# Performance work log

Measured on AMD Instinct MI355X. Metric: run time of the kernel, lower is better.

## Reference

```python
import jax, jax.numpy as jnp
import numpy as np

LAYERS = [3, 1024, 512, 256, 128, 1]
WIDTHS = [3, 1024, 1024, 1024, 1024, 1]  # width per BsPINN: 2^(i-1)*Layers[i]
N = 131072


def _mask(num_blocks, bs1, bs2):
    # block-diagonal mask of ones, built statically (constant under jit)
    return jnp.asarray(np.kron(np.eye(num_blocks, dtype=np.float32),
                               np.ones((bs1, bs2), dtype=np.float32)))


def _xavier(key, shape, fan_in, fan_out):
    lim = np.sqrt(6.0 / (fan_in + fan_out)).astype(np.float32)
    return jax.random.uniform(key, shape, jnp.float32, -lim, lim)


def setup_inputs() -> dict:
    key = jax.random.key(0)
    ks = jax.random.split(key, 6)
    inp = {
        "X": jax.random.uniform(ks[0], (N, 3), dtype=jnp.float32),
        "lb_X": jnp.zeros((3,), jnp.float32),
        "ub_X": jnp.ones((3,), jnp.float32),
    }
    for i in range(5):
        # xavier scale per sub-block Layers[i] x Layers[i+1], as in the torch init
        inp[f"W{i}"] = _xavier(ks[i + 1], (WIDTHS[i], WIDTHS[i + 1]),
                               LAYERS[i], LAYERS[i + 1])
        inp[f"b{i}"] = jnp.zeros((1, WIDTHS[i + 1]), jnp.float32)
    return inp


def reference(X, lb_X, ub_X, W0, b0, W1, b1, W2, b2, W3, b3, W4, b4):
    # masks for hidden layers l=2,3: 2 blocks of 512x512, 4 blocks of 256x256
    m2 = _mask(2, LAYERS[2], 2 * LAYERS[3])   # [1024,1024]
    m3 = _mask(4, LAYERS[3], 2 * LAYERS[4])   # [1024,1024]
    h = 2.0 * (X - lb_X) / (ub_X - lb_X) - 1.0  # [N,3]
    h = jnp.sin(h @ W0 + b0)            # [N,1024] dense
    h = jnp.sin(h @ W1 + b1)            # [N,1024] dense
    h = jnp.sin(h @ (W2 * m2) + b2)     # [N,1024] block-diag (2 blocks)
    h = jnp.sin(h @ (W3 * m3) + b3)     # [N,1024] block-diag (4 blocks)
    return h @ W4 + b4                  # [N,1]
```

## Files before the change

kernel.cpp:

```cpp
#include <hip/hip_runtime.h>

typedef _Float16 f16x8 __attribute__((ext_vector_type(8)));
typedef _Float16 f16x4 __attribute__((ext_vector_type(4)));
typedef __fp16  fp16x2 __attribute__((ext_vector_type(2)));
typedef float f32x4 __attribute__((ext_vector_type(4)));
typedef unsigned int u32;

#define N_TOTAL 131072
#define INV2PI 0.15915494309189535f

__device__ __forceinline__ float fast_sin_revs(float t) {
  return __builtin_amdgcn_sinf(__builtin_amdgcn_fractf(t));
}

__global__ __launch_bounds__(512) void pack_weights(
    const float* __restrict__ W1, const float* __restrict__ W2,
    const float* __restrict__ W3, _Float16* __restrict__ WF1,
    _Float16* __restrict__ WF2, _Float16* __restrict__ WF3) {
  int t = blockIdx.x * 512 + threadIdx.x;
  const float* src; _Float16* dst; int idx, ct, kt, lane, kbase;
  if (t < 131072) {
    idx = t; src = W1; dst = WF1;
    ct = idx >> 11; kt = (idx >> 6) & 31; lane = idx & 63; kbase = 0;
  } else if (t < 196608) {
    idx = t - 131072; src = W2; dst = WF2;
    ct = idx >> 10; kt = (idx >> 6) & 15; lane = idx & 63;
    kbase = (ct >= 32) ? 512 : 0;
  } else {
    idx = t - 196608; src = W3; dst = WF3;
    ct = idx >> 9; kt = (idx >> 6) & 7; lane = idx & 63;
    kbase = (ct >> 4) << 8;
  }
  int c  = ct * 16 + (lane & 15);
  int k0 = kbase + kt * 32 + ((lane >> 4) << 3);
  f16x8 v;
#pragma unroll
  for (int j = 0; j < 8; ++j) v[j] = (_Float16)src[(size_t)(k0 + j) * 1024 + c];
  *reinterpret_cast<f16x8*>(dst + (size_t)idx * 8) = v;
}

template <int KTFULL>
__device__ __forceinline__ void kloop(const _Float16* __restrict__ WF, char* hbr,
                                      f32x4 (&acc)[4][4], int ct0, int lane,
                                      int nkt, int ktW0, u32 ldsk0) {
  const f16x8* wf = reinterpret_cast<const f16x8*>(WF);
  const int arow = lane & 15;
  const int koff = (lane >> 4) << 3;
  const u32 abase = (u32)(arow * 1024);
  const u32 axor  = (u32)((arow & 7) << 4);
  const u32 wbase = (u32)((ct0 * KTFULL + ktW0) * 64 + lane);
#pragma unroll 1
  for (int kt = 0; kt < nkt; ++kt) {
    f16x8 w[4];
#pragma unroll
    for (int cf = 0; cf < 4; ++cf)
      w[cf] = wf[wbase + (u32)(cf * KTFULL) * 64u + (u32)kt * 64u];
    u32 kb = ldsk0 + (u32)(kt * 64) + (u32)(koff * 2);
    f16x8 h[4];
#pragma unroll
    for (int rf = 0; rf < 4; ++rf) {
      u32 addr = ((u32)(rf * 16384) + abase + kb) ^ axor;
      h[rf] = *reinterpret_cast<const f16x8*>(hbr + addr);
    }
    __builtin_amdgcn_s_setprio(1);
#pragma unroll
    for (int cf = 0; cf < 4; ++cf)
#pragma unroll
      for (int rf = 0; rf < 4; ++rf)
        acc[cf][rf] = __builtin_amdgcn_mfma_f32_16x16x32_f16(w[cf], h[rf],
                                                             acc[cf][rf], 0, 0, 0);
    __builtin_amdgcn_s_setprio(0);
  }
}

__global__
__attribute__((amdgpu_flat_work_group_size(1024, 1024), amdgpu_waves_per_eu(4, 4)))
void bspinn_fused(
    const float* __restrict__ X, const float* __restrict__ lb,
    const float* __restrict__ ub,
    const float* __restrict__ W0, const float* __restrict__ b0,
    const _Float16* __restrict__ WF1, const float* __restrict__ b1,
    const _Float16* __restrict__ WF2, const float* __restrict__ b2,
    const _Float16* __restrict__ WF3, const float* __restrict__ b3,
    const float* __restrict__ W4, float* __restrict__ P) {
  __shared__ alignas(16) char hb[128 * 1024];
  __shared__ float xs[128 * 4];
  __shared__ float partials[16 * 128];

  const int tid  = threadIdx.x;
  const int lane = tid & 63;
  const int wid  = tid >> 6;
  const int tile = blockIdx.x >> 1;
  const int half = blockIdx.x & 1;
  const int r0   = tile * 128;

  if (tid < 384) {
    int r = tid / 3, j = tid - r * 3;
    float x = X[(size_t)r0 * 3 + tid];
    xs[r * 4 + j] = 2.0f * (x - lb[j]) / (ub[j] - lb[j]) - 1.0f;
  }

  const int cwave = wid & 7;
  const int rgrp  = wid >> 3;
  char* hbr = hb + rgrp * (64 * 1024);
  const int ct0 = half * 32 + cwave * 4;

  auto layer1 = [&](int cbase) {
    int c1 = tid & 511;
    int rb = (tid >> 9) * 64;
    int cg = cbase + c1;
    float w0v = W0[cg] * INV2PI, w1v = W0[1024 + cg] * INV2PI;
    float w2v = W0[2048 + cg] * INV2PI, bv = b0[cg] * INV2PI;
#pragma unroll 4
    for (int rr = 0; rr < 64; ++rr) {
      int r = rb + rr;
      float x0 = xs[r * 4], x1 = xs[r * 4 + 1], x2 = xs[r * 4 + 2];
      float v = fast_sin_revs(fmaf(x2, w2v, fmaf(x1, w1v, fmaf(x0, w0v, bv))));
      u32 addr = ((u32)(r * 1024 + c1 * 2)) ^ ((u32)((r & 7) << 4));
      *reinterpret_cast<_Float16*>(hb + addr) = (_Float16)v;
    }
  };

  f32x4 acc[4][4];
  auto zacc = [&]() {
#pragma unroll
    for (int cf = 0; cf < 4; ++cf)
#pragma unroll
      for (int rf = 0; rf < 4; ++rf) acc[cf][rf] = f32x4{0.f, 0.f, 0.f, 0.f};
  };

  auto epi = [&](const float* bias) {
    const int csub = (lane >> 4) << 2;
    const int rr = lane & 15;
#pragma unroll
    for (int cf = 0; cf < 4; ++cf) {
      int cg = half * 512 + cwave * 64 + cf * 16 + csub;
      int cl = cwave * 64 + cf * 16 + csub;
      f32x4 bb = *reinterpret_cast<const f32x4*>(bias + cg);
      f32x4 bc;
#pragma unroll
      for (int i = 0; i < 4; ++i) bc[i] = bb[i] * INV2PI;
#pragma unroll
      for (int rf = 0; rf < 4; ++rf) {
        int r = rf * 16 + rr;
        float s0 = fast_sin_revs(fmaf(acc[cf][rf][0], INV2PI, bc[0]));
        float s1 = fast_sin_revs(fmaf(acc[cf][rf][1], INV2PI, bc[1]));
        float s2 = fast_sin_revs(fmaf(acc[cf][rf][2], INV2PI, bc[2]));
        float s3 = fast_sin_revs(fmaf(acc[cf][rf][3], INV2PI, bc[3]));
        union { fp16x2 h2[2]; f16x4 v; } pk;
        pk.h2[0] = __builtin_amdgcn_cvt_pkrtz(s0, s1);
        pk.h2[1] = __builtin_amdgcn_cvt_pkrtz(s2, s3);
        u32 addr = ((u32)(r * 1024 + cl * 2)) ^ ((u32)((r & 7) << 4));
        *reinterpret_cast<f16x4*>(hbr + addr) = pk.v;
      }
    }
  };

  __syncthreads();
  layer1(0);
  __syncthreads();

  zacc();
  kloop<32>(WF1, hbr, acc, ct0, lane, 16, 0, 0);
  __syncthreads();
  layer1(512);
  __syncthreads();
  kloop<32>(WF1, hbr, acc, ct0, lane, 16, 16, 0);
  __syncthreads();
  epi(b1);
  __syncthreads();

  zacc();
  kloop<16>(WF2, hbr, acc, ct0, lane, 16, 0, 0);
  __syncthreads();
  epi(b2);
  __syncthreads();

  zacc();
  kloop<8>(WF3, hbr, acc, ct0, lane, 8, 0, (u32)((cwave >> 2) * 512));
  __syncthreads();
  epi(b3);
  __syncthreads();

  {
    int seg = wid;
    u32 xr = (u32)((lane & 7) << 4);
    float s0 = 0.f, s1 = 0.f;
#pragma unroll
    for (int kk = 0; kk < 32; kk += 8) {
      int kl = seg * 32 + kk;
      const float* w4p = W4 + half * 512 + kl;
      f16x8 v0 = *reinterpret_cast<const f16x8*>(hb + (((u32)(lane * 1024 + kl * 2)) ^ xr));
      f16x8 v1 = *reinterpret_cast<const f16x8*>(hb + (((u32)((lane + 64) * 1024 + kl * 2)) ^ xr));
#pragma unroll
      for (int j = 0; j < 8; ++j) {
        float wv = w4p[j];
        s0 = fmaf((float)v0[j], wv, s0);
        s1 = fmaf((float)v1[j], wv, s1);
      }
    }
    partials[seg * 128 + lane]      = s0;
    partials[seg * 128 + lane + 64] = s1;
  }
  __syncthreads();
  if (tid < 128) {
    float s = 0.f;
#pragma unroll
    for (int g = 0; g < 16; ++g) s += partials[g * 128 + tid];
    P[(size_t)half * N_TOTAL + r0 + tid] = s;
  }
}

__global__ __launch_bounds__(256) void reduce_out(
    const float* __restrict__ P, const float* __restrict__ b4,
    float* __restrict__ out) {
  int i = blockIdx.x * 256 + threadIdx.x;
  out[i] = P[i] + P[N_TOTAL + i] + b4[0];
}

extern "C" void kernel_launch(void* const* d_in, const int* in_sizes, int n_in,
                              void* d_out, int out_size, void* d_ws, size_t ws_size,
                              hipStream_t stream) {
  const float* X  = (const float*)d_in[0];
  const float* lb = (const float*)d_in[1];
  const float* ub = (const float*)d_in[2];
  const float* W0 = (const float*)d_in[3];
  const float* b0 = (const float*)d_in[4];
  const float* W1 = (const float*)d_in[5];
  const float* b1 = (const float*)d_in[6];
  const float* W2 = (const float*)d_in[7];
  const float* b2 = (const float*)d_in[8];
  const float* W3 = (const float*)d_in[9];
  const float* b3 = (const float*)d_in[10];
  const float* W4 = (const float*)d_in[11];
  const float* b4 = (const float*)d_in[12];
  float* out = (float*)d_out;

  _Float16* WF1 = (_Float16*)d_ws;
  _Float16* WF2 = (_Float16*)((char*)d_ws + 2097152);
  _Float16* WF3 = (_Float16*)((char*)d_ws + 3145728);
  float*    P   = (float*)((char*)d_ws + 3670016);

  hipLaunchKernelGGL(pack_weights, dim3(448), dim3(512), 0, stream,
                     W1, W2, W3, WF1, WF2, WF3);
  hipLaunchKernelGGL(bspinn_fused, dim3((N_TOTAL / 128) * 2), dim3(1024), 0, stream,
                     X, lb, ub, W0, b0, WF1, b1, WF2, b2, WF3, b3, W4, P);
  hipLaunchKernelGGL(reduce_out, dim3(N_TOTAL / 256), dim3(256), 0, stream,
                     P, b4, out);
}
```

Baseline: 528.7 us.

## Split fused MLP into 64-row, 512-thread blocks with cheaper sine and swizzle

Halves the work-group from 128 rows and 1024 threads to 64 rows and 512 threads, using 64KB of LDS. This lets two independent blocks share a CU so their barrier phases can overlap instead of all 16 waves stalling on one barrier. It also replaces the fract-plus-scaled-sin sequence with __sinf on the raw argument, widens the LDS XOR swizzle to 16 rows, and writes layer-1 activations as packed half pairs. Dropping the fract range reduction may cost accuracy for large pre-activations, and each block now reuses the global weight traffic across fewer rows.

Measured after the change: 482.6 us, median of 2. -8.7%, faster.

```diff
diff --git a/kernel.cpp b/kernel.cpp
--- a/kernel.cpp
+++ b/kernel.cpp
@@ -7,11 +7,6 @@
 typedef unsigned int u32;
 
 #define N_TOTAL 131072
-#define INV2PI 0.15915494309189535f
-
-__device__ __forceinline__ float fast_sin_revs(float t) {
-  return __builtin_amdgcn_sinf(__builtin_amdgcn_fractf(t));
-}
 
 __global__ __launch_bounds__(512) void pack_weights(
     const float* __restrict__ W1, const float* __restrict__ W2,
@@ -40,27 +35,28 @@
 }
 
 template <int KTFULL>
-__device__ __forceinline__ void kloop(const _Float16* __restrict__ WF, char* hbr,
+__device__ __forceinline__ void kloop(const _Float16* __restrict__ WF, char* hb,
                                       f32x4 (&acc)[4][4], int ct0, int lane,
                                       int nkt, int ktW0, u32 ldsk0) {
-  const f16x8* wf = reinterpret_cast<const f16x8*>(WF);
+  const f16x8* wf = reinterpret_cast<const f16x8*>(WF) +
+                    (u32)((ct0 * KTFULL + ktW0) * 64 + lane);
   const int arow = lane & 15;
   const int koff = (lane >> 4) << 3;
   const u32 abase = (u32)(arow * 1024);
-  const u32 axor  = (u32)((arow & 7) << 4);
-  const u32 wbase = (u32)((ct0 * KTFULL + ktW0) * 64 + lane);
+  const u32 axor  = (u32)(arow << 4);
+
 #pragma unroll 1
   for (int kt = 0; kt < nkt; ++kt) {
     f16x8 w[4];
 #pragma unroll
     for (int cf = 0; cf < 4; ++cf)
-      w[cf] = wf[wbase + (u32)(cf * KTFULL) * 64u + (u32)kt * 64u];
+      w[cf] = wf[(u32)(cf * KTFULL) * 64u + (u32)kt * 64u];
     u32 kb = ldsk0 + (u32)(kt * 64) + (u32)(koff * 2);
     f16x8 h[4];
 #pragma unroll
     for (int rf = 0; rf < 4; ++rf) {
       u32 addr = ((u32)(rf * 16384) + abase + kb) ^ axor;
-      h[rf] = *reinterpret_cast<const f16x8*>(hbr + addr);
+      h[rf] = *reinterpret_cast<const f16x8*>(hb + addr);
     }
     __builtin_amdgcn_s_setprio(1);
 #pragma unroll
@@ -74,7 +70,7 @@
 }
 
 __global__
-__attribute__((amdgpu_flat_work_group_size(1024, 1024), amdgpu_waves_per_eu(4, 4)))
+__attribute__((amdgpu_flat_work_group_size(512, 512), amdgpu_waves_per_eu(4, 4)))
 void bspinn_fused(
     const float* __restrict__ X, const float* __restrict__ lb,
     const float* __restrict__ ub,
@@ -83,130 +79,122 @@
     const _Float16* __restrict__ WF2, const float* __restrict__ b2,
     const _Float16* __restrict__ WF3, const float* __restrict__ b3,
     const float* __restrict__ W4, float* __restrict__ P) {
-  __shared__ alignas(16) char hb[128 * 1024];
-  __shared__ float xs[128 * 4];
-  __shared__ float partials[16 * 128];
+  __shared__ alignas(16) char hb[64 * 1024];
+  __shared__ float xs[64 * 4];
+  __shared__ float partials[8 * 64];
 
   const int tid  = threadIdx.x;
   const int lane = tid & 63;
   const int wid  = tid >> 6;
   const int tile = blockIdx.x >> 1;
   const int half = blockIdx.x & 1;
-  const int r0   = tile * 128;
-
-  if (tid < 384) {
+  const int r0   = tile * 64;
+
+  if (tid < 192) {
     int r = tid / 3, j = tid - r * 3;
     float x = X[(size_t)r0 * 3 + tid];
     xs[r * 4 + j] = 2.0f * (x - lb[j]) / (ub[j] - lb[j]) - 1.0f;
   }
-
-  const int cwave = wid & 7;
-  const int rgrp  = wid >> 3;
-  char* hbr = hb + rgrp * (64 * 1024);
-  const int ct0 = half * 32 + cwave * 4;
+  __syncthreads();
 
   auto layer1 = [&](int cbase) {
-    int c1 = tid & 511;
-    int rb = (tid >> 9) * 64;
-    int cg = cbase + c1;
-    float w0v = W0[cg] * INV2PI, w1v = W0[1024 + cg] * INV2PI;
-    float w2v = W0[2048 + cg] * INV2PI, bv = b0[cg] * INV2PI;
+    int c0l = (tid & 255) * 2;
+    int rb  = (tid >> 8) * 32;
+    int cg  = cbase + c0l;
+    float wa0 = W0[cg],        wb0 = W0[cg + 1];
+    float wa1 = W0[1024 + cg], wb1 = W0[1025 + cg];
+    float wa2 = W0[2048 + cg], wb2 = W0[2049 + cg];
+    float ba = b0[cg], bbv = b0[cg + 1];
 #pragma unroll 4
-    for (int rr = 0; rr < 64; ++rr) {
-      int r = rb + rr;
+    for (int rr2 = 0; rr2 < 32; ++rr2) {
+      int r = rb + rr2;
       float x0 = xs[r * 4], x1 = xs[r * 4 + 1], x2 = xs[r * 4 + 2];
-      float v = fast_sin_revs(fmaf(x2, w2v, fmaf(x1, w1v, fmaf(x0, w0v, bv))));
-      u32 addr = ((u32)(r * 1024 + c1 * 2)) ^ ((u32)((r & 7) << 4));
-      *reinterpret_cast<_Float16*>(hb + addr) = (_Float16)v;
+      float va = __sinf(fmaf(x2, wa2, fmaf(x1, wa1, fmaf(x0, wa0, ba))));
+      float vb = __sinf(fmaf(x2, wb2, fmaf(x1, wb1, fmaf(x0, wb0, bbv))));
+      union { fp16x2 h2; u32 u; } pk;
+      pk.h2 = __builtin_amdgcn_cvt_pkrtz(va, vb);
+      u32 addr = ((u32)(r * 1024 + c0l * 2)) ^ ((u32)((r & 15) << 4));
+      *reinterpret_cast<u32*>(hb + addr) = pk.u;
     }
   };
 
+  const int csub = (lane >> 4) << 2;
+  const int rr   = lane & 15;
+  const int ct0  = half * 32 + wid * 4;
   f32x4 acc[4][4];
+
   auto zacc = [&]() {
 #pragma unroll
     for (int cf = 0; cf < 4; ++cf)
 #pragma unroll
       for (int rf = 0; rf < 4; ++rf) acc[cf][rf] = f32x4{0.f, 0.f, 0.f, 0.f};
   };
-
-  auto epi = [&](const float* bias) {
-    const int csub = (lane >> 4) << 2;
-    const int rr = lane & 15;
+  auto epi_store = [&](const float* bias) {
 #pragma unroll
     for (int cf = 0; cf < 4; ++cf) {
-      int cg = half * 512 + cwave * 64 + cf * 16 + csub;
-      int cl = cwave * 64 + cf * 16 + csub;
+      int c0l = wid * 64 + cf * 16 + csub;
+      int cg  = half * 512 + c0l;
       f32x4 bb = *reinterpret_cast<const f32x4*>(bias + cg);
-      f32x4 bc;
-#pragma unroll
-      for (int i = 0; i < 4; ++i) bc[i] = bb[i] * INV2PI;
 #pragma unroll
       for (int rf = 0; rf < 4; ++rf) {
         int r = rf * 16 + rr;
-        float s0 = fast_sin_revs(fmaf(acc[cf][rf][0], INV2PI, bc[0]));
-        float s1 = fast_sin_revs(fmaf(acc[cf][rf][1], INV2PI, bc[1]));
-        float s2 = fast_sin_revs(fmaf(acc[cf][rf][2], INV2PI, bc[2]));
-        float s3 = fast_sin_revs(fmaf(acc[cf][rf][3], INV2PI, bc[3]));
+        float s0 = __sinf(acc[cf][rf][0] + bb[0]);
+        float s1 = __sinf(acc[cf][rf][1] + bb[1]);
+        float s2 = __sinf(acc[cf][rf][2] + bb[2]);
+        float s3 = __sinf(acc[cf][rf][3] + bb[3]);
         union { fp16x2 h2[2]; f16x4 v; } pk;
         pk.h2[0] = __builtin_amdgcn_cvt_pkrtz(s0, s1);
         pk.h2[1] = __builtin_amdgcn_cvt_pkrtz(s2, s3);
-        u32 addr = ((u32)(r * 1024 + cl * 2)) ^ ((u32)((r & 7) << 4));
-        *reinterpret_cast<f16x4*>(hbr + addr) = pk.v;
+        u32 addr = ((u32)(r * 1024 + c0l * 2)) ^ ((u32)(rr << 4));
+        *reinterpret_cast<f16x4*>(hb + addr) = pk.v;
       }
     }
   };
 
-  __syncthreads();
   layer1(0);
   __syncthreads();
-
   zacc();
-  kloop<32>(WF1, hbr, acc, ct0, lane, 16, 0, 0);
+  kloop<32>(WF1, hb, acc, ct0, lane, 16, 0, 0);
   __syncthreads();
   layer1(512);
   __syncthreads();
-  kloop<32>(WF1, hbr, acc, ct0, lane, 16, 16, 0);
-  __syncthreads();
-  epi(b1);
+  kloop<32>(WF1, hb, acc, ct0, lane, 16, 16, 0);
+  __syncthreads();
+  epi_store(b1);
   __syncthreads();
 
   zacc();
-  kloop<16>(WF2, hbr, acc, ct0, lane, 16, 0, 0);
-  __syncthreads();
-  epi(b2);
+  kloop<16>(WF2, hb, acc, ct0, lane, 16, 0, 0);
+  __syncthreads();
+  epi_store(b2);
   __syncthreads();
 
   zacc();
-  kloop<8>(WF3, hbr, acc, ct0, lane, 8, 0, (u32)((cwave >> 2) * 512));
-  __syncthreads();
-  epi(b3);
+  kloop<8>(WF3, hb, acc, ct0, lane, 8, 0, (u32)((wid >> 2) * 512));
+  __syncthreads();
+  epi_store(b3);
   __syncthreads();
 
   {
-    int seg = wid;
-    u32 xr = (u32)((lane & 7) << 4);
-    float s0 = 0.f, s1 = 0.f;
-#pragma unroll
-    for (int kk = 0; kk < 32; kk += 8) {
-      int kl = seg * 32 + kk;
+    int r = lane;
+    u32 rb = (u32)(r * 1024);
+    u32 xr = (u32)((r & 15) << 4);
+    float s = 0.f;
+#pragma unroll
+    for (int kk = 0; kk < 64; kk += 8) {
+      int kl = wid * 64 + kk;
       const float* w4p = W4 + half * 512 + kl;
-      f16x8 v0 = *reinterpret_cast<const f16x8*>(hb + (((u32)(lane * 1024 + kl * 2)) ^ xr));
-      f16x8 v1 = *reinterpret_cast<const f16x8*>(hb + (((u32)((lane + 64) * 1024 + kl * 2)) ^ xr));
-#pragma unroll
-      for (int j = 0; j < 8; ++j) {
-        float wv = w4p[j];
-        s0 = fmaf((float)v0[j], wv, s0);
-        s1 = fmaf((float)v1[j], wv, s1);
-      }
-    }
-    partials[seg * 128 + lane]      = s0;
-    partials[seg * 128 + lane + 64] = s1;
-  }
-  __syncthreads();
-  if (tid < 128) {
+      f16x8 v = *reinterpret_cast<const f16x8*>(hb + ((rb + (u32)(kl * 2)) ^ xr));
+#pragma unroll
+      for (int j = 0; j < 8; ++j) s = fmaf((float)v[j], w4p[j], s);
+    }
+    partials[wid * 64 + r] = s;
+  }
+  __syncthreads();
+  if (tid < 64) {
     float s = 0.f;
 #pragma unroll
-    for (int g = 0; g < 16; ++g) s += partials[g * 128 + tid];
+    for (int g = 0; g < 8; ++g) s += partials[g * 64 + tid];
     P[(size_t)half * N_TOTAL + r0 + tid] = s;
   }
 }
@@ -243,7 +231,7 @@
 
   hipLaunchKernelGGL(pack_weights, dim3(448), dim3(512), 0, stream,
                      W1, W2, W3, WF1, WF2, WF3);
-  hipLaunchKernelGGL(bspinn_fused, dim3((N_TOTAL / 128) * 2), dim3(1024), 0, stream,
+  hipLaunchKernelGGL(bspinn_fused, dim3((N_TOTAL / 64) * 2), dim3(512), 0, stream,
                      X, lb, ub, W0, b0, WF1, b1, WF2, b2, WF3, b3, W4, P);
   hipLaunchKernelGGL(reduce_out, dim3(N_TOTAL / 256), dim3(256), 0, stream,
                      P, b4, out);
```
